# Performance work log

Hardware: AMD Instinct MI355X
Metric: run time of the kernel (lower is better)

The kernel has to match this reference:

```python
import jax, jax.numpy as jnp
import numpy as np

B, M, D, H = 64, 1024, 1024, 8
HD = D // H
MID = [128, 64, 128]
CELU_ALPHA = 1.3
GN_EPS = 1e-5


def _proj(x, W, b, g, beta):
    # Linear -> CELU(1.3) -> GroupNorm(H groups, affine) on 2D input [N, D]
    y = jax.nn.celu(x @ W + b, alpha=CELU_ALPHA)
    y = y.reshape(-1, H, HD)
    mu = y.mean(-1, keepdims=True)
    var = ((y - mu) ** 2).mean(-1, keepdims=True)
    y = (y - mu) * jax.lax.rsqrt(var + GN_EPS)
    return y * g.reshape(H, HD) + beta.reshape(H, HD)  # [N, H, HD]


def _forward(query, key, mask, value1, value2,
             W_q, b_q, g_q, beta_q, W_k, b_k, g_k, beta_k,
             W_v1, b_v1, g_v1, beta_v1, W_v2, b_v2, g_v2, beta_v2,
             W1, b1, Wl, bl, Wl2, bl2):
    q = _proj(query, W_q, b_q, g_q, beta_q)          # [B,H,hd]
    v1 = _proj(value1, W_v1, b_v1, g_v1, beta_v1)    # [B,H,hd]
    k = _proj(key.reshape(-1, D), W_k, b_k, g_k, beta_k).reshape(B, M, H, HD).transpose(0, 2, 1, 3)    # [B,H,M,hd]
    v2 = _proj(value2.reshape(-1, D), W_v2, b_v2, g_v2, beta_v2).reshape(B, M, H, HD).transpose(0, 2, 1, 3)
    # cosine similarity (torch eps=1e-8) and normalized query direction (F.normalize eps=1e-12)
    qn = jnp.linalg.norm(q, axis=-1)                 # [B,H]
    kn = jnp.linalg.norm(k, axis=-1)                 # [B,H,M]
    dot = jnp.einsum('bhd,bhmd->bhm', q, k)
    cos = dot / (jnp.maximum(qn[..., None], 1e-8) * jnp.maximum(kn, 1e-8))
    q_dir = q / jnp.maximum(qn, 1e-12)[..., None]
    score = cos[..., None] * q_dir[:, :, None, :]    # [B,H,M,hd] rank-1 outer product
    # SCAtt attention net (dropout inactive in eval)
    am = jax.nn.relu(score @ W1 + b1)                # [B,H,M,mid]
    m = mask[:, None, :]                             # [B,1,M]
    pool = (am * m[..., None]).sum(2) / m.sum(2)[..., None]   # [B,H,mid] masked mean over M
    a_sp = (am @ Wl + bl)[..., 0]                    # [B,H,M]
    a_sp = jnp.where(m == 0, -1e9, a_sp)
    a_sp = jax.nn.softmax(a_sp, axis=-1)
    a_ch = jax.nn.sigmoid(pool @ Wl2 + bl2)          # [B,H,hd] channel gate
    v2o = jnp.einsum('bhm,bhmd->bhd', a_sp, v2)      # spatial aggregation
    attn = v1 * v2o * a_ch                           # [B,H,hd]
    return attn.reshape(B, H * HD)


def setup_inputs() -> dict:
    rng = jax.random.key(0)
    ks = jax.random.split(rng, 16)
    s = 0.02
    inp = {
        'query': jax.random.normal(ks[0], (B, D), jnp.float32),
        'key': jax.random.normal(ks[1], (B, M, D), jnp.float32),
        'mask': jnp.ones((B, M), jnp.float32),
        'value1': jax.random.normal(ks[2], (B, D), jnp.float32),
        'value2': jax.random.normal(ks[3], (B, M, D), jnp.float32),
    }
    i = 4
    for name in ['q', 'k', 'v1', 'v2']:
        inp['W_' + name] = jax.random.normal(ks[i], (D, D), jnp.float32) * s; i += 1
        inp['b_' + name] = jnp.zeros((D,), jnp.float32)
        inp['g_' + name] = jnp.ones((D,), jnp.float32)
        inp['beta_' + name] = jnp.zeros((D,), jnp.float32)
    inp['W1'] = jax.random.normal(ks[i], (MID[0], MID[1]), jnp.float32) * s; i += 1
    inp['b1'] = jnp.zeros((MID[1],), jnp.float32)
    inp['Wl'] = jax.random.normal(ks[i], (MID[1], 1), jnp.float32) * s; i += 1
    inp['bl'] = jnp.zeros((1,), jnp.float32)
    inp['Wl2'] = jax.random.normal(ks[i], (MID[1], MID[2]), jnp.float32) * s; i += 1
    inp['bl2'] = jnp.zeros((MID[2],), jnp.float32)
    return inp


def reference(query, key, mask, value1, value2,
              W_q, b_q, g_q, beta_q, W_k, b_k, g_k, beta_k,
              W_v1, b_v1, g_v1, beta_v1, W_v2, b_v2, g_v2, beta_v2,
              W1, b1, Wl, bl, Wl2, bl2):
    return _forward(query, key, mask, value1, value2,
                    W_q, b_q, g_q, beta_q, W_k, b_k, g_k, beta_k,
                    W_v1, b_v1, g_v1, beta_v1, W_v2, b_v2, g_v2, beta_v2,
                    W1, b1, Wl, bl, Wl2, bl2)
```

## Files before the change

### kernel.cpp

```cpp
#include <hip/hip_runtime.h>
#include <hip/hip_bf16.h>

#define B_  64
#define M_  1024
#define D_  1024
#define H_  8
#define HD_ 128
#define BM_ (B_*M_)

#define CELU_A  1.3f
#define CELU_IA 0.7692307692307693f
#define GN_EPSF 1e-5f

typedef float floatx4 __attribute__((ext_vector_type(4)));
typedef __bf16 bf16x8 __attribute__((ext_vector_type(8)));

__device__ __forceinline__ void gload_lds16(const void* g, void* l) {
    __builtin_amdgcn_global_load_lds((const __attribute__((address_space(1))) void*)g,
                                     (__attribute__((address_space(3))) void*)l, 16, 0, 0);
}

__device__ __forceinline__ float celu_f(float x) {
    return x > 0.f ? x : (CELU_A * __expf(x * CELU_IA) - CELU_A);
}

__global__ void transpose_convert(const float* __restrict__ W0, const float* __restrict__ W1m,
                                  __bf16* __restrict__ T0, __bf16* __restrict__ T1) {
    __shared__ float tile[32][33];
    int id = blockIdx.x;
    const float* W = (id < 1024) ? W0 : W1m;
    __bf16* T = (id < 1024) ? T0 : T1;
    id &= 1023;
    int bx = id & 31, by = id >> 5;
    int tx = threadIdx.x & 31, ty = threadIdx.x >> 5;
    #pragma unroll
    for (int i = 0; i < 32; i += 8)
        tile[ty + i][tx] = W[(size_t)(by*32 + ty + i) * D_ + bx*32 + tx];
    __syncthreads();
    #pragma unroll
    for (int i = 0; i < 32; i += 8)
        T[(size_t)(bx*32 + ty + i) * D_ + by*32 + tx] = (__bf16)tile[tx][ty + i];
}

__global__ void proj_small(const float* __restrict__ x, const float* __restrict__ W,
                           const float* __restrict__ bias, const float* __restrict__ g,
                           const float* __restrict__ beta, float* __restrict__ out,
                           float* __restrict__ qn_out, const float* __restrict__ W1,
                           float* __restrict__ qw1, int extras) {
    __shared__ float sX[D_];
    __shared__ float sred[4];
    __shared__ float sQd[HD_];
    const int bh = blockIdx.x;
    const int b = bh >> 3, h = bh & 7;
    const int tid = threadIdx.x;

    #pragma unroll
    for (int i = 0; i < D_/128; i++) sX[i*128 + tid] = x[(size_t)b*D_ + i*128 + tid];
    __syncthreads();

    const int col = h*HD_ + tid;
    float acc = bias[col];
    const float* Wp = W + col;
    #pragma unroll 16
    for (int d = 0; d < D_; d++) acc = fmaf(sX[d], Wp[(size_t)d*D_], acc);

    float y = celu_f(acc);

    float s1 = y, s2 = y*y;
    #pragma unroll
    for (int off = 1; off < 64; off <<= 1) { s1 += __shfl_xor(s1, off, 64); s2 += __shfl_xor(s2, off, 64); }
    if ((tid & 63) == 0) { sred[tid >> 6] = s1; sred[2 + (tid >> 6)] = s2; }
    __syncthreads();
    s1 = sred[0] + sred[1]; s2 = sred[2] + sred[3];
    float mu = s1 * (1.f/HD_);
    float var = fmaxf(s2 * (1.f/HD_) - mu*mu, 0.f);
    float rstd = rsqrtf(var + GN_EPSF);
    float k = (y - mu) * rstd * g[col] + beta[col];
    out[(size_t)b*D_ + col] = k;

    if (extras) {
        __syncthreads();
        float q2 = k*k;
        #pragma unroll
        for (int off = 1; off < 64; off <<= 1) q2 += __shfl_xor(q2, off, 64);
        if ((tid & 63) == 0) sred[tid >> 6] = q2;
        __syncthreads();
        float qn = sqrtf(sred[0] + sred[1]);
        if (tid == 0) qn_out[bh] = qn;
        sQd[tid] = k / fmaxf(qn, 1e-12f);
        __syncthreads();
        if (tid < 64) {
            float s = 0.f;
            #pragma unroll 16
            for (int d2 = 0; d2 < HD_; d2++) s = fmaf(sQd[d2], W1[d2*64 + tid], s);
            qw1[bh*64 + tid] = s;
        }
    }
}

#define TM 128
#define BK 32
#define ASTR 40

#define GEMM_CORE(Aptr, Btptr)                                                          \
    const int tid = threadIdx.x;                                                        \
    const int h = blockIdx.x & 7;                                                       \
    const int row0 = (blockIdx.x >> 3) * TM;                                            \
    const int b = row0 >> 10;                                                           \
    const int col0 = h * HD_;                                                           \
    const int lane = tid & 63;                                                          \
    const int wv = tid >> 6;                                                            \
    const int wrow = wv >> 1, wcol = wv & 1;                                            \
    const int quad = lane >> 4, l15 = lane & 15;                                        \
    floatx4 acc[4][4];                                                                  \
    {   floatx4 z = {0.f, 0.f, 0.f, 0.f};                                               \
        _Pragma("unroll") for (int i = 0; i < 4; i++)                                   \
        _Pragma("unroll") for (int j = 0; j < 4; j++) acc[i][j] = z;  }                 \
    const int ar = tid >> 1;                                                            \
    const int ak = (tid & 1) << 4;                                                      \
    const float* Ap = Aptr + (size_t)(row0 + ar) * D_ + ak;                             \
    const __bf16* Bp0 = Btptr + (size_t)(col0 + (tid >> 2)) * D_ + ((tid & 3) << 3);    \
    const __bf16* Bp1 = Btptr + (size_t)(col0 + 64 + (tid >> 2)) * D_ + ((tid & 3) << 3);\
    __bf16* Bd0 = Bs + tid * 8;                                                         \
    __bf16* Bd1 = Bs + (tid + 256) * 8;                                                 \
    for (int k0 = 0; k0 < D_; k0 += BK) {                                               \
        __syncthreads();                                                                \
        gload_lds16(Bp0 + k0, Bd0);                                                     \
        gload_lds16(Bp1 + k0, Bd1);                                                     \
        {                                                                               \
            const float* p = Ap + k0;                                                   \
            floatx4 f0 = *(const floatx4*)p;                                            \
            floatx4 f1 = *(const floatx4*)(p + 4);                                      \
            floatx4 f2 = *(const floatx4*)(p + 8);                                      \
            floatx4 f3 = *(const floatx4*)(p + 12);                                     \
            bf16x8 u0, u1;                                                              \
            _Pragma("unroll") for (int i = 0; i < 4; i++) {                             \
                u0[i] = (__bf16)f0[i]; u0[i+4] = (__bf16)f1[i];                         \
                u1[i] = (__bf16)f2[i]; u1[i+4] = (__bf16)f3[i]; }                       \
            *(bf16x8*)(As + ar*ASTR + ak)     = u0;                                     \
            *(bf16x8*)(As + ar*ASTR + ak + 8) = u1;                                     \
        }                                                                               \
        __syncthreads();                                                                \
        bf16x8 fa[4], fb[4];                                                            \
        _Pragma("unroll") for (int i = 0; i < 4; i++)                                   \
            fa[i] = *(const bf16x8*)(As + (wrow*64 + i*16 + l15)*ASTR + quad*8);        \
        _Pragma("unroll") for (int i = 0; i < 4; i++)                                   \
            fb[i] = *(const bf16x8*)(Bs + (wcol*64 + i*16 + l15)*BK + quad*8);          \
        _Pragma("unroll") for (int mi = 0; mi < 4; mi++)                                \
        _Pragma("unroll") for (int ni = 0; ni < 4; ni++)                                \
            acc[mi][ni] = __builtin_amdgcn_mfma_f32_16x16x32_bf16(fa[mi], fb[ni],       \
                                                                  acc[mi][ni], 0, 0, 0);\
    }

__global__ __launch_bounds__(256, 2) void gemm_key(
    const float* __restrict__ A, const __bf16* __restrict__ Bt,
    const float* __restrict__ bias, const float* __restrict__ gv,
    const float* __restrict__ betav, const float* __restrict__ qv,
    float* __restrict__ dotv, float* __restrict__ knv) {
    __shared__ __attribute__((aligned(16))) __bf16 As[TM * ASTR];
    __shared__ __attribute__((aligned(16))) __bf16 Bs[TM * BK];
    __shared__ float red0[2][TM], red1[2][TM], redD[2][TM], redK[2][TM];

    GEMM_CORE(A, Bt)

    float biasc[4], gc[4], bc[4], qc[4];
    #pragma unroll
    for (int ni = 0; ni < 4; ni++) {
        int c = col0 + wcol*64 + ni*16 + l15;
        biasc[ni] = bias[c]; gc[ni] = gv[c]; bc[ni] = betav[c];
        qc[ni] = qv[(size_t)b*D_ + c];
    }
    #pragma unroll
    for (int mi = 0; mi < 4; mi++)
    #pragma unroll
    for (int ni = 0; ni < 4; ni++)
    #pragma unroll
    for (int r = 0; r < 4; r++)
        acc[mi][ni][r] = celu_f(acc[mi][ni][r] + biasc[ni]);

    #pragma unroll
    for (int mi = 0; mi < 4; mi++)
    #pragma unroll
    for (int r = 0; r < 4; r++) {
        float s1 = 0.f, s2 = 0.f;
        #pragma unroll
        for (int ni = 0; ni < 4; ni++) { float v = acc[mi][ni][r]; s1 += v; s2 += v*v; }
        #pragma unroll
        for (int off = 1; off < 16; off <<= 1) { s1 += __shfl_xor(s1, off, 16); s2 += __shfl_xor(s2, off, 16); }
        if (l15 == 0) { int rr = wrow*64 + mi*16 + quad*4 + r; red0[wcol][rr] = s1; red1[wcol][rr] = s2; }
    }
    __syncthreads();
    #pragma unroll
    for (int mi = 0; mi < 4; mi++)
    #pragma unroll
    for (int r = 0; r < 4; r++) {
        int rr = wrow*64 + mi*16 + quad*4 + r;
        float s1 = red0[0][rr] + red0[1][rr];
        float s2 = red1[0][rr] + red1[1][rr];
        float mu = s1 * (1.f/HD_);
        float var = fmaxf(s2 * (1.f/HD_) - mu*mu, 0.f);
        float rstd = rsqrtf(var + GN_EPSF);
        float dp = 0.f, kp = 0.f;
        #pragma unroll
        for (int ni = 0; ni < 4; ni++) {
            float kk = (acc[mi][ni][r] - mu) * rstd * gc[ni] + bc[ni];
            dp = fmaf(kk, qc[ni], dp);
            kp = fmaf(kk, kk, kp);
        }
        #pragma unroll
        for (int off = 1; off < 16; off <<= 1) { dp += __shfl_xor(dp, off, 16); kp += __shfl_xor(kp, off, 16); }
        if (l15 == 0) { redD[wcol][rr] = dp; redK[wcol][rr] = kp; }
    }
    __syncthreads();
    if (tid < TM) {
        int gr = row0 + tid;
        size_t oi = ((size_t)(b*H_ + h)) * M_ + (gr & (M_ - 1));
        dotv[oi] = redD[0][tid] + redD[1][tid];
        knv[oi]  = sqrtf(redK[0][tid] + redK[1][tid]);
    }
}

__global__ __launch_bounds__(256, 2) void gemm_v2(
    const float* __restrict__ A, const __bf16* __restrict__ Bt,
    const float* __restrict__ bias, const float* __restrict__ gv,
    const float* __restrict__ betav, const float* __restrict__ asp,
    float* __restrict__ v2o) {
    __shared__ __attribute__((aligned(16))) __bf16 As[TM * ASTR];
    __shared__ __attribute__((aligned(16))) __bf16 Bs[TM * BK];
    __shared__ float red0[2][TM], red1[2][TM];
    __shared__ float sAsp[TM];

    GEMM_CORE(A, Bt)

    if (tid < TM) {
        int gr = row0 + tid;
        sAsp[tid] = asp[((size_t)(b*H_ + h)) * M_ + (gr & (M_ - 1))];
    }
    float biasc[4], gc[4], bc[4];
    #pragma unroll
    for (int ni = 0; ni < 4; ni++) {
        int c = col0 + wcol*64 + ni*16 + l15;
        biasc[ni] = bias[c]; gc[ni] = gv[c]; bc[ni] = betav[c];
    }
    #pragma unroll
    for (int mi = 0; mi < 4; mi++)
    #pragma unroll
    for (int ni = 0; ni < 4; ni++)
    #pragma unroll
    for (int r = 0; r < 4; r++)
        acc[mi][ni][r] = celu_f(acc[mi][ni][r] + biasc[ni]);

    #pragma unroll
    for (int mi = 0; mi < 4; mi++)
    #pragma unroll
    for (int r = 0; r < 4; r++) {
        float s1 = 0.f, s2 = 0.f;
        #pragma unroll
        for (int ni = 0; ni < 4; ni++) { float v = acc[mi][ni][r]; s1 += v; s2 += v*v; }
        #pragma unroll
        for (int off = 1; off < 16; off <<= 1) { s1 += __shfl_xor(s1, off, 16); s2 += __shfl_xor(s2, off, 16); }
        if (l15 == 0) { int rr = wrow*64 + mi*16 + quad*4 + r; red0[wcol][rr] = s1; red1[wcol][rr] = s2; }
    }
    __syncthreads();
    float cs[4] = {0.f, 0.f, 0.f, 0.f};
    #pragma unroll
    for (int mi = 0; mi < 4; mi++)
    #pragma unroll
    for (int r = 0; r < 4; r++) {
        int rr = wrow*64 + mi*16 + quad*4 + r;
        float s1 = red0[0][rr] + red0[1][rr];
        float s2 = red1[0][rr] + red1[1][rr];
        float mu = s1 * (1.f/HD_);
        float var = fmaxf(s2 * (1.f/HD_) - mu*mu, 0.f);
        float rstd = rsqrtf(var + GN_EPSF);
        float w = sAsp[rr];
        #pragma unroll
        for (int ni = 0; ni < 4; ni++) {
            float vv = (acc[mi][ni][r] - mu) * rstd * gc[ni] + bc[ni];
            cs[ni] = fmaf(w, vv, cs[ni]);
        }
    }
    #pragma unroll
    for (int ni = 0; ni < 4; ni++) {
        cs[ni] += __shfl_xor(cs[ni], 16, 64);
        cs[ni] += __shfl_xor(cs[ni], 32, 64);
    }
    if (quad == 0) {
        #pragma unroll
        for (int ni = 0; ni < 4; ni++)
            atomicAdd(&v2o[(size_t)b*D_ + col0 + wcol*64 + ni*16 + l15], cs[ni]);
    }
}

__global__ __launch_bounds__(256) void attn_small(
    const float* __restrict__ dotv, const float* __restrict__ knv,
    const float* __restrict__ qn_in, const float* __restrict__ qw1,
    const float* __restrict__ b1, const float* __restrict__ Wl,
    const float* __restrict__ bl, const float* __restrict__ Wl2,
    const float* __restrict__ bl2, const float* __restrict__ mask,
    float* __restrict__ asp, float* __restrict__ ach) {
    __shared__ float sqw[64], sb1[64], sWl[64];
    __shared__ float sredA[4], sredB[4], sMsum[4];
    __shared__ float sPool[4][64];
    __shared__ float sPoolF[64];
    const int bh = blockIdx.x;
    const int b = bh >> 3;
    const int tid = threadIdx.x, lane = tid & 63, wv = tid >> 6;
    if (tid < 64) { sqw[tid] = qw1[bh*64 + tid]; sb1[tid] = b1[tid]; sWl[tid] = Wl[tid]; }
    __syncthreads();
    const float rqn = 1.f / fmaxf(qn_in[bh], 1e-8f);
    const float blv = bl[0];
    const size_t base = (size_t)bh * M_;
    float pacc[64];
    #pragma unroll
    for (int j = 0; j < 64; j++) pacc[j] = 0.f;
    float lg[4], e[4];
    float msum = 0.f;
    #pragma unroll
    for (int i = 0; i < 4; i++) {
        int m = i*256 + tid;
        float kn = fmaxf(knv[base + m], 1e-8f);
        float cosv = dotv[base + m] * rqn / kn;
        float mk = mask[(size_t)b*M_ + m];
        msum += mk;
        float l = blv;
        #pragma unroll
        for (int j = 0; j < 64; j++) {
            float a = fmaxf(fmaf(cosv, sqw[j], sb1[j]), 0.f);
            l = fmaf(a, sWl[j], l);
            pacc[j] = fmaf(a, mk, pacc[j]);
        }
        lg[i] = (mk == 0.f) ? -1e9f : l;
    }
    #pragma unroll
    for (int off = 1; off < 64; off <<= 1) msum += __shfl_xor(msum, off, 64);
    if (lane == 0) sMsum[wv] = msum;
    float lm = fmaxf(fmaxf(lg[0], lg[1]), fmaxf(lg[2], lg[3]));
    #pragma unroll
    for (int off = 1; off < 64; off <<= 1) lm = fmaxf(lm, __shfl_xor(lm, off, 64));
    if (lane == 0) sredA[wv] = lm;
    __syncthreads();
    float gmax = fmaxf(fmaxf(sredA[0], sredA[1]), fmaxf(sredA[2], sredA[3]));
    float mtot = sMsum[0] + sMsum[1] + sMsum[2] + sMsum[3];
    float es = 0.f;
    #pragma unroll
    for (int i = 0; i < 4; i++) { e[i] = __expf(lg[i] - gmax); es += e[i]; }
    #pragma unroll
    for (int off = 1; off < 64; off <<= 1) es += __shfl_xor(es, off, 64);
    if (lane == 0) sredB[wv] = es;
    #pragma unroll
    for (int j = 0; j < 64; j++) {
        float p = pacc[j];
        #pragma unroll
        for (int off = 1; off < 64; off <<= 1) p += __shfl_xor(p, off, 64);
        if (lane == 0) sPool[wv][j] = p;
    }
    __syncthreads();
    float inv_etot = 1.f / (sredB[0] + sredB[1] + sredB[2] + sredB[3]);
    #pragma unroll
    for (int i = 0; i < 4; i++) asp[base + i*256 + tid] = e[i] * inv_etot;
    if (tid < 64)
        sPoolF[tid] = (sPool[0][tid] + sPool[1][tid] + sPool[2][tid] + sPool[3][tid]) / mtot;
    __syncthreads();
    if (tid < 128) {
        float z = bl2[tid];
        #pragma unroll 8
        for (int j = 0; j < 64; j++) z = fmaf(sPoolF[j], Wl2[j*128 + tid], z);
        ach[(size_t)bh*HD_ + tid] = 1.f / (1.f + __expf(-z));
    }
}

__global__ void final_mul(const float* __restrict__ v1, const float* __restrict__ v2o,
                          const float* __restrict__ ach, float* __restrict__ out) {
    int i = blockIdx.x*256 + threadIdx.x;
    out[i] = v1[i] * v2o[i] * ach[i];
}

extern "C" void kernel_launch(void* const* d_in, const int* in_sizes, int n_in,
                              void* d_out, int out_size, void* d_ws, size_t ws_size,
                              hipStream_t stream) {
    (void)in_sizes; (void)n_in; (void)out_size; (void)ws_size;
    const float* query  = (const float*)d_in[0];
    const float* key    = (const float*)d_in[1];
    const float* mask   = (const float*)d_in[2];
    const float* value1 = (const float*)d_in[3];
    const float* value2 = (const float*)d_in[4];
    const float* W_q = (const float*)d_in[5];  const float* b_q = (const float*)d_in[6];
    const float* g_q = (const float*)d_in[7];  const float* beta_q = (const float*)d_in[8];
    const float* W_k = (const float*)d_in[9];  const float* b_k = (const float*)d_in[10];
    const float* g_k = (const float*)d_in[11]; const float* beta_k = (const float*)d_in[12];
    const float* W_v1 = (const float*)d_in[13]; const float* b_v1 = (const float*)d_in[14];
    const float* g_v1 = (const float*)d_in[15]; const float* beta_v1 = (const float*)d_in[16];
    const float* W_v2 = (const float*)d_in[17]; const float* b_v2 = (const float*)d_in[18];
    const float* g_v2 = (const float*)d_in[19]; const float* beta_v2 = (const float*)d_in[20];
    const float* W1  = (const float*)d_in[21]; const float* b1  = (const float*)d_in[22];
    const float* Wl  = (const float*)d_in[23]; const float* bl  = (const float*)d_in[24];
    const float* Wl2 = (const float*)d_in[25]; const float* bl2 = (const float*)d_in[26];

    char* p = (char*)d_ws;
    auto alloc = [&](size_t bytes) { char* r = p; p += (bytes + 255) & ~(size_t)255; return r; };
    __bf16* WkT   = (__bf16*)alloc((size_t)D_*D_*sizeof(__bf16));
    __bf16* Wv2T  = (__bf16*)alloc((size_t)D_*D_*sizeof(__bf16));
    float* qbuf   = (float*)alloc((size_t)B_*D_*4);
    float* v1buf  = (float*)alloc((size_t)B_*D_*4);
    float* qnb    = (float*)alloc((size_t)B_*H_*4);
    float* qw1b   = (float*)alloc((size_t)B_*H_*64*4);
    float* dotb   = (float*)alloc((size_t)B_*H_*M_*4);
    float* knb    = (float*)alloc((size_t)B_*H_*M_*4);
    float* aspb   = (float*)alloc((size_t)B_*H_*M_*4);
    float* achb   = (float*)alloc((size_t)B_*D_*4);
    float* v2ob   = (float*)alloc((size_t)B_*D_*4);

    hipMemsetAsync(v2ob, 0, (size_t)B_*D_*4, stream);
    transpose_convert<<<2048, 256, 0, stream>>>(W_k, W_v2, WkT, Wv2T);
    proj_small<<<B_*H_, 128, 0, stream>>>(query, W_q, b_q, g_q, beta_q, qbuf, qnb, W1, qw1b, 1);
    proj_small<<<B_*H_, 128, 0, stream>>>(value1, W_v1, b_v1, g_v1, beta_v1, v1buf, nullptr, nullptr, nullptr, 0);
    gemm_key<<<(BM_/TM)*(D_/HD_), 256, 0, stream>>>(key, WkT, b_k, g_k, beta_k, qbuf, dotb, knb);
    attn_small<<<B_*H_, 256, 0, stream>>>(dotb, knb, qnb, qw1b, b1, Wl, bl, Wl2, bl2, mask, aspb, achb);
    gemm_v2<<<(BM_/TM)*(D_/HD_), 256, 0, stream>>>(value2, Wv2T, b_v2, g_v2, beta_v2, aspb, v2ob);
    final_mul<<<(B_*D_)/256, 256, 0, stream>>>(v1buf, v2ob, achb, (float*)d_out);
}
```

Measured before the change: 1.151 ms.

## Pre-pack activations and weights into MFMA fragment-order bf16 tiles before GEMMs

Adds a prep_A pass that converts the fp32 key/value2 activations to bf16 in fragment-ordered 128x32 tiles, and a prep_W pass that packs weights the same way. The GEMM cores can then load both operands with direct global-to-LDS copies and conflict-free contiguous fragment reads, instead of converting fp32 in registers each k-step. Block ordering is remapped for L2 reuse and occupancy is raised to 3 blocks per SM. The cost is an extra full read of the activations plus a bf16 write and re-read, chunked to fit the workspace.

```diff
diff --git a/kernel.cpp b/kernel.cpp
--- a/kernel.cpp
+++ b/kernel.cpp
@@ -7,6 +7,7 @@
 #define H_  8
 #define HD_ 128
 #define BM_ (B_*M_)
+#define NRT_ (BM_/128)
 
 #define CELU_A  1.3f
 #define CELU_IA 0.7692307692307693f
@@ -24,22 +25,233 @@
     return x > 0.f ? x : (CELU_A * __expf(x * CELU_IA) - CELU_A);
 }
 
-__global__ void transpose_convert(const float* __restrict__ W0, const float* __restrict__ W1m,
-                                  __bf16* __restrict__ T0, __bf16* __restrict__ T1) {
-    __shared__ float tile[32][33];
-    int id = blockIdx.x;
-    const float* W = (id < 1024) ? W0 : W1m;
-    __bf16* T = (id < 1024) ? T0 : T1;
-    id &= 1023;
-    int bx = id & 31, by = id >> 5;
-    int tx = threadIdx.x & 31, ty = threadIdx.x >> 5;
-    #pragma unroll
-    for (int i = 0; i < 32; i += 8)
-        tile[ty + i][tx] = W[(size_t)(by*32 + ty + i) * D_ + bx*32 + tx];
-    __syncthreads();
-    #pragma unroll
-    for (int i = 0; i < 32; i += 8)
-        T[(size_t)(bx*32 + ty + i) * D_ + by*32 + tx] = (__bf16)tile[tx][ty + i];
+__device__ __forceinline__ int frag_pos(int r, int c) {
+    return (((r >> 6) * 256 + ((r >> 4) & 3) * 64 + (c >> 3) * 16 + (r & 15)) << 3) + (c & 7);
+}
+
+__global__ void prep_W(const float* __restrict__ Wk, const float* __restrict__ Wv2,
+                       __bf16* __restrict__ out) {
+    __shared__ __attribute__((aligned(16))) __bf16 sT[4096];
+    const int id = blockIdx.x;
+    const float* W = (id < 256) ? Wk : Wv2;
+    const int ht = id & 255;
+    const int h = ht >> 5, t = ht & 31;
+    const int tid = threadIdx.x;
+    #pragma unroll
+    for (int it = 0; it < 4; it++) {
+        int fid = it * 256 + tid;
+        int kl = fid >> 5;
+        int c4 = fid & 31;
+        floatx4 v = *(const floatx4*)(W + (size_t)(t * 32 + kl) * D_ + h * HD_ + c4 * 4);
+        #pragma unroll
+        for (int e = 0; e < 4; e++) {
+            int c = c4 * 4 + e;
+            sT[frag_pos(c, kl)] = (__bf16)v[e];
+        }
+    }
+    __syncthreads();
+    __bf16* o = out + (size_t)id * 4096;
+    *(bf16x8*)(o + tid * 8)        = *(const bf16x8*)(sT + tid * 8);
+    *(bf16x8*)(o + 2048 + tid * 8) = *(const bf16x8*)(sT + 2048 + tid * 8);
+}
+
+__global__ void prep_A(const float* __restrict__ src, __bf16* __restrict__ out, int rt0) {
+    __shared__ __attribute__((aligned(16))) __bf16 sT[4096];
+    const int rtL = blockIdx.x;
+    const int rt = rt0 + rtL;
+    const int tid = threadIdx.x;
+    for (int t = 0; t < 32; t++) {
+        #pragma unroll
+        for (int it = 0; it < 4; it++) {
+            int fid = it * 256 + tid;
+            int r = fid >> 3;
+            int c4 = fid & 7;
+            floatx4 v = *(const floatx4*)(src + (size_t)(rt * 128 + r) * D_ + t * 32 + c4 * 4);
+            #pragma unroll
+            for (int e = 0; e < 4; e++) sT[frag_pos(r, c4 * 4 + e)] = (__bf16)v[e];
+        }
+        __syncthreads();
+        __bf16* o = out + (size_t)(rtL * 32 + t) * 4096;
+        *(bf16x8*)(o + tid * 8)        = *(const bf16x8*)(sT + tid * 8);
+        *(bf16x8*)(o + 2048 + tid * 8) = *(const bf16x8*)(sT + 2048 + tid * 8);
+        __syncthreads();
+    }
+}
+
+#define GEMM_CORE2(ATp, BTp)                                                            \
+    const int tid = threadIdx.x;                                                        \
+    const int n = blockIdx.x;                                                           \
+    const int rtL = ((n >> 6) << 3) | (n & 7);                                          \
+    const int h = (n >> 3) & 7;                                                         \
+    const int rt = rt0 + rtL;                                                           \
+    const int b = rt >> 3;                                                              \
+    const int col0 = h * HD_;                                                           \
+    const int lane = tid & 63;                                                          \
+    const int wv = tid >> 6;                                                            \
+    const int wrow = wv >> 1, wcol = wv & 1;                                            \
+    const int quad = lane >> 4, l15 = lane & 15;                                        \
+    floatx4 acc[4][4];                                                                  \
+    {   floatx4 z = {0.f, 0.f, 0.f, 0.f};                                               \
+        _Pragma("unroll") for (int i = 0; i < 4; i++)                                   \
+        _Pragma("unroll") for (int j = 0; j < 4; j++) acc[i][j] = z;  }                 \
+    const __bf16* Ab = ATp + (size_t)rtL * 32 * 4096 + tid * 8;                         \
+    const __bf16* Bb = BTp + (size_t)h * 32 * 4096 + tid * 8;                           \
+    for (int t = 0; t < 32; t++) {                                                      \
+        __syncthreads();                                                                \
+        gload_lds16(Ab + t * 4096,        As + tid * 8);                                \
+        gload_lds16(Ab + t * 4096 + 2048, As + 2048 + tid * 8);                         \
+        gload_lds16(Bb + t * 4096,        Bs + tid * 8);                                \
+        gload_lds16(Bb + t * 4096 + 2048, Bs + 2048 + tid * 8);                         \
+        __syncthreads();                                                                \
+        bf16x8 fa[4], fb[4];                                                            \
+        _Pragma("unroll") for (int i = 0; i < 4; i++)                                   \
+            fa[i] = *(const bf16x8*)(As + wrow * 2048 + i * 512 + lane * 8);            \
+        _Pragma("unroll") for (int i = 0; i < 4; i++)                                   \
+            fb[i] = *(const bf16x8*)(Bs + wcol * 2048 + i * 512 + lane * 8);            \
+        _Pragma("unroll") for (int mi = 0; mi < 4; mi++)                                \
+        _Pragma("unroll") for (int ni = 0; ni < 4; ni++)                                \
+            acc[mi][ni] = __builtin_amdgcn_mfma_f32_16x16x32_bf16(fa[mi], fb[ni],       \
+                                                                  acc[mi][ni], 0, 0, 0);\
+    }
+
+__global__ __launch_bounds__(256, 3) void gemm_key(
+    const __bf16* __restrict__ AT, const __bf16* __restrict__ BT,
+    const float* __restrict__ bias, const float* __restrict__ gv,
+    const float* __restrict__ betav, const float* __restrict__ qv,
+    float* __restrict__ dotv, float* __restrict__ knv, int rt0) {
+    __shared__ __attribute__((aligned(16))) __bf16 As[4096];
+    __shared__ __attribute__((aligned(16))) __bf16 Bs[4096];
+    __shared__ float red0[2][128], red1[2][128], redD[2][128], redK[2][128];
+
+    GEMM_CORE2(AT, BT)
+
+    float biasc[4], gc[4], bc[4], qc[4];
+    #pragma unroll
+    for (int ni = 0; ni < 4; ni++) {
+        int c = col0 + wcol*64 + ni*16 + l15;
+        biasc[ni] = bias[c]; gc[ni] = gv[c]; bc[ni] = betav[c];
+        qc[ni] = qv[(size_t)b*D_ + c];
+    }
+    #pragma unroll
+    for (int mi = 0; mi < 4; mi++)
+    #pragma unroll
+    for (int ni = 0; ni < 4; ni++)
+    #pragma unroll
+    for (int r = 0; r < 4; r++)
+        acc[mi][ni][r] = celu_f(acc[mi][ni][r] + biasc[ni]);
+
+    #pragma unroll
+    for (int mi = 0; mi < 4; mi++)
+    #pragma unroll
+    for (int r = 0; r < 4; r++) {
+        float s1 = 0.f, s2 = 0.f;
+        #pragma unroll
+        for (int ni = 0; ni < 4; ni++) { float v = acc[mi][ni][r]; s1 += v; s2 += v*v; }
+        #pragma unroll
+        for (int off = 1; off < 16; off <<= 1) { s1 += __shfl_xor(s1, off, 16); s2 += __shfl_xor(s2, off, 16); }
+        if (l15 == 0) { int rr = wrow*64 + mi*16 + quad*4 + r; red0[wcol][rr] = s1; red1[wcol][rr] = s2; }
+    }
+    __syncthreads();
+    #pragma unroll
+    for (int mi = 0; mi < 4; mi++)
+    #pragma unroll
+    for (int r = 0; r < 4; r++) {
+        int rr = wrow*64 + mi*16 + quad*4 + r;
+        float s1 = red0[0][rr] + red0[1][rr];
+        float s2 = red1[0][rr] + red1[1][rr];
+        float mu = s1 * (1.f/HD_);
+        float var = fmaxf(s2 * (1.f/HD_) - mu*mu, 0.f);
+        float rstd = rsqrtf(var + GN_EPSF);
+        float dp = 0.f, kp = 0.f;
+        #pragma unroll
+        for (int ni = 0; ni < 4; ni++) {
+            float kk = (acc[mi][ni][r] - mu) * rstd * gc[ni] + bc[ni];
+            dp = fmaf(kk, qc[ni], dp);
+            kp = fmaf(kk, kk, kp);
+        }
+        #pragma unroll
+        for (int off = 1; off < 16; off <<= 1) { dp += __shfl_xor(dp, off, 16); kp += __shfl_xor(kp, off, 16); }
+        if (l15 == 0) { redD[wcol][rr] = dp; redK[wcol][rr] = kp; }
+    }
+    __syncthreads();
+    if (tid < 128) {
+        int gr = rt * 128 + tid;
+        size_t oi = ((size_t)(b*H_ + h)) * M_ + (gr & (M_ - 1));
+        dotv[oi] = redD[0][tid] + redD[1][tid];
+        knv[oi]  = sqrtf(redK[0][tid] + redK[1][tid]);
+    }
+}
+
+__global__ __launch_bounds__(256, 3) void gemm_v2(
+    const __bf16* __restrict__ AT, const __bf16* __restrict__ BT,
+    const float* __restrict__ bias, const float* __restrict__ gv,
+    const float* __restrict__ betav, const float* __restrict__ asp,
+    float* __restrict__ v2o, int rt0) {
+    __shared__ __attribute__((aligned(16))) __bf16 As[4096];
+    __shared__ __attribute__((aligned(16))) __bf16 Bs[4096];
+    __shared__ float red0[2][128], red1[2][128];
+    __shared__ float sAsp[128];
+
+    GEMM_CORE2(AT, BT)
+
+    if (tid < 128) {
+        int gr = rt * 128 + tid;
+        sAsp[tid] = asp[((size_t)(b*H_ + h)) * M_ + (gr & (M_ - 1))];
+    }
+    float biasc[4], gc[4], bc[4];
+    #pragma unroll
+    for (int ni = 0; ni < 4; ni++) {
+        int c = col0 + wcol*64 + ni*16 + l15;
+        biasc[ni] = bias[c]; gc[ni] = gv[c]; bc[ni] = betav[c];
+    }
+    #pragma unroll
+    for (int mi = 0; mi < 4; mi++)
+    #pragma unroll
+    for (int ni = 0; ni < 4; ni++)
+    #pragma unroll
+    for (int r = 0; r < 4; r++)
+        acc[mi][ni][r] = celu_f(acc[mi][ni][r] + biasc[ni]);
+
+    #pragma unroll
+    for (int mi = 0; mi < 4; mi++)
+    #pragma unroll
+    for (int r = 0; r < 4; r++) {
+        float s1 = 0.f, s2 = 0.f;
+        #pragma unroll
+        for (int ni = 0; ni < 4; ni++) { float v = acc[mi][ni][r]; s1 += v; s2 += v*v; }
+        #pragma unroll
+        for (int off = 1; off < 16; off <<= 1) { s1 += __shfl_xor(s1, off, 16); s2 += __shfl_xor(s2, off, 16); }
+        if (l15 == 0) { int rr = wrow*64 + mi*16 + quad*4 + r; red0[wcol][rr] = s1; red1[wcol][rr] = s2; }
+    }
+    __syncthreads();
+    float cs[4] = {0.f, 0.f, 0.f, 0.f};
+    #pragma unroll
+    for (int mi = 0; mi < 4; mi++)
+    #pragma unroll
+    for (int r = 0; r < 4; r++) {
+        int rr = wrow*64 + mi*16 + quad*4 + r;
+        float s1 = red0[0][rr] + red0[1][rr];
+        float s2 = red1[0][rr] + red1[1][rr];
+        float mu = s1 * (1.f/HD_);
+        float var = fmaxf(s2 * (1.f/HD_) - mu*mu, 0.f);
+        float rstd = rsqrtf(var + GN_EPSF);
+        float w = sAsp[rr];
+        #pragma unroll
+        for (int ni = 0; ni < 4; ni++) {
+            float vv = (acc[mi][ni][r] - mu) * rstd * gc[ni] + bc[ni];
+            cs[ni] = fmaf(w, vv, cs[ni]);
+        }
+    }
+    #pragma unroll
+    for (int ni = 0; ni < 4; ni++) {
+        cs[ni] += __shfl_xor(cs[ni], 16, 64);
+        cs[ni] += __shfl_xor(cs[ni], 32, 64);
+    }
+    if (quad == 0) {
+        #pragma unroll
+        for (int ni = 0; ni < 4; ni++)
+            atomicAdd(&v2o[(size_t)b*D_ + col0 + wcol*64 + ni*16 + l15], cs[ni]);
+    }
 }
 
 __global__ void proj_small(const float* __restrict__ x, const float* __restrict__ W,
@@ -95,200 +307,6 @@
             for (int d2 = 0; d2 < HD_; d2++) s = fmaf(sQd[d2], W1[d2*64 + tid], s);
             qw1[bh*64 + tid] = s;
         }
-    }
-}
-
-#define TM 128
-#define BK 32
-#define ASTR 40
-
-#define GEMM_CORE(Aptr, Btptr)                                                          \
-    const int tid = threadIdx.x;                                                        \
-    const int h = blockIdx.x & 7;                                                       \
-    const int row0 = (blockIdx.x >> 3) * TM;                                            \
-    const int b = row0 >> 10;                                                           \
-    const int col0 = h * HD_;                                                           \
-    const int lane = tid & 63;                                                          \
-    const int wv = tid >> 6;                                                            \
-    const int wrow = wv >> 1, wcol = wv & 1;                                            \
-    const int quad = lane >> 4, l15 = lane & 15;                                        \
-    floatx4 acc[4][4];                                                                  \
-    {   floatx4 z = {0.f, 0.f, 0.f, 0.f};                                               \
-        _Pragma("unroll") for (int i = 0; i < 4; i++)                                   \
-        _Pragma("unroll") for (int j = 0; j < 4; j++) acc[i][j] = z;  }                 \
-    const int ar = tid >> 1;                                                            \
-    const int ak = (tid & 1) << 4;                                                      \
-    const float* Ap = Aptr + (size_t)(row0 + ar) * D_ + ak;                             \
-    const __bf16* Bp0 = Btptr + (size_t)(col0 + (tid >> 2)) * D_ + ((tid & 3) << 3);    \
-    const __bf16* Bp1 = Btptr + (size_t)(col0 + 64 + (tid >> 2)) * D_ + ((tid & 3) << 3);\
-    __bf16* Bd0 = Bs + tid * 8;                                                         \
-    __bf16* Bd1 = Bs + (tid + 256) * 8;                                                 \
-    for (int k0 = 0; k0 < D_; k0 += BK) {                                               \
-        __syncthreads();                                                                \
-        gload_lds16(Bp0 + k0, Bd0);                                                     \
-        gload_lds16(Bp1 + k0, Bd1);                                                     \
-        {                                                                               \
-            const float* p = Ap + k0;                                                   \
-            floatx4 f0 = *(const floatx4*)p;                                            \
-            floatx4 f1 = *(const floatx4*)(p + 4);                                      \
-            floatx4 f2 = *(const floatx4*)(p + 8);                                      \
-            floatx4 f3 = *(const floatx4*)(p + 12);                                     \
-            bf16x8 u0, u1;                                                              \
-            _Pragma("unroll") for (int i = 0; i < 4; i++) {                             \
-                u0[i] = (__bf16)f0[i]; u0[i+4] = (__bf16)f1[i];                         \
-                u1[i] = (__bf16)f2[i]; u1[i+4] = (__bf16)f3[i]; }                       \
-            *(bf16x8*)(As + ar*ASTR + ak)     = u0;                                     \
-            *(bf16x8*)(As + ar*ASTR + ak + 8) = u1;                                     \
-        }                                                                               \
-        __syncthreads();                                                                \
-        bf16x8 fa[4], fb[4];                                                            \
-        _Pragma("unroll") for (int i = 0; i < 4; i++)                                   \
-            fa[i] = *(const bf16x8*)(As + (wrow*64 + i*16 + l15)*ASTR + quad*8);        \
-        _Pragma("unroll") for (int i = 0; i < 4; i++)                                   \
-            fb[i] = *(const bf16x8*)(Bs + (wcol*64 + i*16 + l15)*BK + quad*8);          \
-        _Pragma("unroll") for (int mi = 0; mi < 4; mi++)                                \
-        _Pragma("unroll") for (int ni = 0; ni < 4; ni++)                                \
-            acc[mi][ni] = __builtin_amdgcn_mfma_f32_16x16x32_bf16(fa[mi], fb[ni],       \
-                                                                  acc[mi][ni], 0, 0, 0);\
-    }
-
-__global__ __launch_bounds__(256, 2) void gemm_key(
-    const float* __restrict__ A, const __bf16* __restrict__ Bt,
-    const float* __restrict__ bias, const float* __restrict__ gv,
-    const float* __restrict__ betav, const float* __restrict__ qv,
-    float* __restrict__ dotv, float* __restrict__ knv) {
-    __shared__ __attribute__((aligned(16))) __bf16 As[TM * ASTR];
-    __shared__ __attribute__((aligned(16))) __bf16 Bs[TM * BK];
-    __shared__ float red0[2][TM], red1[2][TM], redD[2][TM], redK[2][TM];
-
-    GEMM_CORE(A, Bt)
-
-    float biasc[4], gc[4], bc[4], qc[4];
-    #pragma unroll
-    for (int ni = 0; ni < 4; ni++) {
-        int c = col0 + wcol*64 + ni*16 + l15;
-        biasc[ni] = bias[c]; gc[ni] = gv[c]; bc[ni] = betav[c];
-        qc[ni] = qv[(size_t)b*D_ + c];
-    }
-    #pragma unroll
-    for (int mi = 0; mi < 4; mi++)
-    #pragma unroll
-    for (int ni = 0; ni < 4; ni++)
-    #pragma unroll
-    for (int r = 0; r < 4; r++)
-        acc[mi][ni][r] = celu_f(acc[mi][ni][r] + biasc[ni]);
-
-    #pragma unroll
-    for (int mi = 0; mi < 4; mi++)
-    #pragma unroll
-    for (int r = 0; r < 4; r++) {
-        float s1 = 0.f, s2 = 0.f;
-        #pragma unroll
-        for (int ni = 0; ni < 4; ni++) { float v = acc[mi][ni][r]; s1 += v; s2 += v*v; }
-        #pragma unroll
-        for (int off = 1; off < 16; off <<= 1) { s1 += __shfl_xor(s1, off, 16); s2 += __shfl_xor(s2, off, 16); }
-        if (l15 == 0) { int rr = wrow*64 + mi*16 + quad*4 + r; red0[wcol][rr] = s1; red1[wcol][rr] = s2; }
-    }
-    __syncthreads();
-    #pragma unroll
-    for (int mi = 0; mi < 4; mi++)
-    #pragma unroll
-    for (int r = 0; r < 4; r++) {
-        int rr = wrow*64 + mi*16 + quad*4 + r;
-        float s1 = red0[0][rr] + red0[1][rr];
-        float s2 = red1[0][rr] + red1[1][rr];
-        float mu = s1 * (1.f/HD_);
-        float var = fmaxf(s2 * (1.f/HD_) - mu*mu, 0.f);
-        float rstd = rsqrtf(var + GN_EPSF);
-        float dp = 0.f, kp = 0.f;
-        #pragma unroll
-        for (int ni = 0; ni < 4; ni++) {
-            float kk = (acc[mi][ni][r] - mu) * rstd * gc[ni] + bc[ni];
-            dp = fmaf(kk, qc[ni], dp);
-            kp = fmaf(kk, kk, kp);
-        }
-        #pragma unroll
-        for (int off = 1; off < 16; off <<= 1) { dp += __shfl_xor(dp, off, 16); kp += __shfl_xor(kp, off, 16); }
-        if (l15 == 0) { redD[wcol][rr] = dp; redK[wcol][rr] = kp; }
-    }
-    __syncthreads();
-    if (tid < TM) {
-        int gr = row0 + tid;
-        size_t oi = ((size_t)(b*H_ + h)) * M_ + (gr & (M_ - 1));
-        dotv[oi] = redD[0][tid] + redD[1][tid];
-        knv[oi]  = sqrtf(redK[0][tid] + redK[1][tid]);
-    }
-}
-
-__global__ __launch_bounds__(256, 2) void gemm_v2(
-    const float* __restrict__ A, const __bf16* __restrict__ Bt,
-    const float* __restrict__ bias, const float* __restrict__ gv,
-    const float* __restrict__ betav, const float* __restrict__ asp,
-    float* __restrict__ v2o) {
-    __shared__ __attribute__((aligned(16))) __bf16 As[TM * ASTR];
-    __shared__ __attribute__((aligned(16))) __bf16 Bs[TM * BK];
-    __shared__ float red0[2][TM], red1[2][TM];
-    __shared__ float sAsp[TM];
-
-    GEMM_CORE(A, Bt)
-
-    if (tid < TM) {
-        int gr = row0 + tid;
-        sAsp[tid] = asp[((size_t)(b*H_ + h)) * M_ + (gr & (M_ - 1))];
-    }
-    float biasc[4], gc[4], bc[4];
-    #pragma unroll
-    for (int ni = 0; ni < 4; ni++) {
-        int c = col0 + wcol*64 + ni*16 + l15;
-        biasc[ni] = bias[c]; gc[ni] = gv[c]; bc[ni] = betav[c];
-    }
-    #pragma unroll
-    for (int mi = 0; mi < 4; mi++)
-    #pragma unroll
-    for (int ni = 0; ni < 4; ni++)
-    #pragma unroll
-    for (int r = 0; r < 4; r++)
-        acc[mi][ni][r] = celu_f(acc[mi][ni][r] + biasc[ni]);
-
-    #pragma unroll
-    for (int mi = 0; mi < 4; mi++)
-    #pragma unroll
-    for (int r = 0; r < 4; r++) {
-        float s1 = 0.f, s2 = 0.f;
-        #pragma unroll
-        for (int ni = 0; ni < 4; ni++) { float v = acc[mi][ni][r]; s1 += v; s2 += v*v; }
-        #pragma unroll
-        for (int off = 1; off < 16; off <<= 1) { s1 += __shfl_xor(s1, off, 16); s2 += __shfl_xor(s2, off, 16); }
-        if (l15 == 0) { int rr = wrow*64 + mi*16 + quad*4 + r; red0[wcol][rr] = s1; red1[wcol][rr] = s2; }
-    }
-    __syncthreads();
-    float cs[4] = {0.f, 0.f, 0.f, 0.f};
-    #pragma unroll
-    for (int mi = 0; mi < 4; mi++)
-    #pragma unroll
-    for (int r = 0; r < 4; r++) {
-        int rr = wrow*64 + mi*16 + quad*4 + r;
-        float s1 = red0[0][rr] + red0[1][rr];
-        float s2 = red1[0][rr] + red1[1][rr];
-        float mu = s1 * (1.f/HD_);
-        float var = fmaxf(s2 * (1.f/HD_) - mu*mu, 0.f);
-        float rstd = rsqrtf(var + GN_EPSF);
-        float w = sAsp[rr];
-        #pragma unroll
-        for (int ni = 0; ni < 4; ni++) {
-            float vv = (acc[mi][ni][r] - mu) * rstd * gc[ni] + bc[ni];
-            cs[ni] = fmaf(w, vv, cs[ni]);
-        }
-    }
-    #pragma unroll
-    for (int ni = 0; ni < 4; ni++) {
-        cs[ni] += __shfl_xor(cs[ni], 16, 64);
-        cs[ni] += __shfl_xor(cs[ni], 32, 64);
-    }
-    if (quad == 0) {
-        #pragma unroll
-        for (int ni = 0; ni < 4; ni++)
-            atomicAdd(&v2o[(size_t)b*D_ + col0 + wcol*64 + ni*16 + l15], cs[ni]);
     }
 }
 
@@ -379,7 +397,7 @@
 extern "C" void kernel_launch(void* const* d_in, const int* in_sizes, int n_in,
                               void* d_out, int out_size, void* d_ws, size_t ws_size,
                               hipStream_t stream) {
-    (void)in_sizes; (void)n_in; (void)out_size; (void)ws_size;
+    (void)in_sizes; (void)n_in; (void)out_size;
     const float* query  = (const float*)d_in[0];
     const float* key    = (const float*)d_in[1];
     const float* mask   = (const float*)d_in[2];
@@ -399,8 +417,7 @@
 
     char* p = (char*)d_ws;
     auto alloc = [&](size_t bytes) { char* r = p; p += (bytes + 255) & ~(size_t)255; return r; };
-    __bf16* WkT   = (__bf16*)alloc((size_t)D_*D_*sizeof(__bf16));
-    __bf16* Wv2T  = (__bf16*)alloc((size_t)D_*D_*sizeof(__bf16));
+    __bf16* Wtiles = (__bf16*)alloc((size_t)2*D_*D_*sizeof(__bf16));
     float* qbuf   = (float*)alloc((size_t)B_*D_*4);
     float* v1buf  = (float*)alloc((size_t)B_*D_*4);
     float* qnb    = (float*)alloc((size_t)B_*H_*4);
@@ -411,12 +428,27 @@
     float* achb   = (float*)alloc((size_t)B_*D_*4);
     float* v2ob   = (float*)alloc((size_t)B_*D_*4);
 
+    size_t used = (size_t)(p - (char*)d_ws);
+    int nrtc = NRT_;
+    while (nrtc > 8 && used + (size_t)nrtc * 32 * 4096 * sizeof(__bf16) > ws_size) nrtc >>= 1;
+    __bf16* Atiles = (__bf16*)alloc((size_t)nrtc * 32 * 4096 * sizeof(__bf16));
+
+    const __bf16* WTk  = Wtiles;
+    const __bf16* WTv2 = Wtiles + (size_t)D_*D_;
+
     hipMemsetAsync(v2ob, 0, (size_t)B_*D_*4, stream);
-    transpose_convert<<<2048, 256, 0, stream>>>(W_k, W_v2, WkT, Wv2T);
+    prep_W<<<512, 256, 0, stream>>>(W_k, W_v2, Wtiles);
     proj_small<<<B_*H_, 128, 0, stream>>>(query, W_q, b_q, g_q, beta_q, qbuf, qnb, W1, qw1b, 1);
     proj_small<<<B_*H_, 128, 0, stream>>>(value1, W_v1, b_v1, g_v1, beta_v1, v1buf, nullptr, nullptr, nullptr, 0);
-    gemm_key<<<(BM_/TM)*(D_/HD_), 256, 0, stream>>>(key, WkT, b_k, g_k, beta_k, qbuf, dotb, knb);
+
+    for (int rt0 = 0; rt0 < NRT_; rt0 += nrtc) {
+        prep_A<<<nrtc, 256, 0, stream>>>(key, Atiles, rt0);
+        gemm_key<<<nrtc*8, 256, 0, stream>>>(Atiles, WTk, b_k, g_k, beta_k, qbuf, dotb, knb, rt0);
+    }
     attn_small<<<B_*H_, 256, 0, stream>>>(dotb, knb, qnb, qw1b, b1, Wl, bl, Wl2, bl2, mask, aspb, achb);
-    gemm_v2<<<(BM_/TM)*(D_/HD_), 256, 0, stream>>>(value2, Wv2T, b_v2, g_v2, beta_v2, aspb, v2ob);
+    for (int rt0 = 0; rt0 < NRT_; rt0 += nrtc) {
+        prep_A<<<nrtc, 256, 0, stream>>>(value2, Atiles, rt0);
+        gemm_v2<<<nrtc*8, 256, 0, stream>>>(Atiles, WTv2, b_v2, g_v2, beta_v2, aspb, v2ob, rt0);
+    }
     final_mul<<<(B_*D_)/256, 256, 0, stream>>>(v1buf, v2ob, achb, (float*)d_out);
 }
```

Result: faster. 1.096 ms (-4.8%).
